# Kernel tuning notes

Measured on AMD Instinct MI355X. Metric: run time of the kernel, lower is better.

Reference implementation:

```python
import jax, jax.numpy as jnp
import numpy as np
import math

D = 1024       # feature_dim
H = 4          # n_heads
HD = D // H
T = 512        # vertice frames
S = 512        # audio frames
V3 = 15069     # vertice_dim (5023*3)
NSUB = 8
PERIOD = 25
MAXLEN = 600
DFF = 2 * D
AUD = 768


def _build_alibi(n_head=H, max_seq=MAXLEN, period=PERIOD):
    def slopes(n):
        def p2(n):
            start = 2 ** (-2 ** (-(math.log2(n) - 3)))
            return [start * start ** i for i in range(n)]
        if math.log2(n).is_integer():
            return p2(n)
        c = 2 ** math.floor(math.log2(n))
        return p2(c) + slopes(2 * c)[0::2][: n - c]
    sl = np.array(slopes(n_head), np.float32)
    bias = (np.arange(0, max_seq, period)[:, None].repeat(period, 1).reshape(-1) // period).astype(np.float32)
    bias = -bias[::-1]
    i = np.arange(max_seq)[:, None]
    j = np.arange(max_seq)[None, :]
    idx = np.clip(max_seq - 1 - i + j, 0, max_seq - 1)
    alibi = np.where(j <= i, bias[idx], 0.0).astype(np.float32)
    causal = np.where(j <= i, 0.0, -np.inf).astype(np.float32)
    return causal[None] + sl[:, None, None] * alibi[None]   # [H, maxlen, maxlen]


def _build_pe(d=D, period=PERIOD, max_seq=MAXLEN):
    pos = np.arange(period, dtype=np.float32)[:, None]
    div = np.exp(np.arange(0, d, 2, dtype=np.float32) * (-math.log(10000.0) / d))
    pe = np.zeros((period, d), np.float32)
    pe[:, 0::2] = np.sin(pos * div)
    pe[:, 1::2] = np.cos(pos * div)
    reps = max_seq // period + 1
    return np.tile(pe, (reps, 1))[None]                     # [1, reps*period, d]

_ALIBI = jnp.asarray(_build_alibi())
_PE = jnp.asarray(_build_pe())


def _ln(x, g, b, eps=1e-5):
    m = jnp.mean(x, -1, keepdims=True)
    v = jnp.mean((x - m) ** 2, -1, keepdims=True)
    return (x - m) * jax.lax.rsqrt(v + eps) * g + b


def _mha(q_in, kv_in, Wqkv, bqkv, Wo, bo, add_mask=None, bool_mask=None):
    # torch nn.MultiheadAttention with in_proj [3D, D]; y = x @ W.T + b
    B, Tq, _ = q_in.shape
    Ts = kv_in.shape[1]
    Wq, Wk, Wv = jnp.split(Wqkv, 3, axis=0)
    bq, bk, bv = jnp.split(bqkv, 3)
    q = (q_in @ Wq.T + bq).reshape(B, Tq, H, HD).transpose(0, 2, 1, 3)
    k = (kv_in @ Wk.T + bk).reshape(B, Ts, H, HD).transpose(0, 2, 1, 3)
    v = (kv_in @ Wv.T + bv).reshape(B, Ts, H, HD).transpose(0, 2, 1, 3)
    scores = jnp.einsum('bhtd,bhsd->bhts', q, k) / math.sqrt(HD)
    if add_mask is not None:
        scores = scores + add_mask[None]            # [1,H,Tq,Ts] float additive (ALiBi+causal)
    if bool_mask is not None:
        scores = jnp.where(bool_mask, -jnp.inf, scores)  # True == masked (torch semantics)
    attn = jax.nn.softmax(scores, axis=-1)
    out = jnp.einsum('bhts,bhsd->bhtd', attn, v).transpose(0, 2, 1, 3).reshape(B, Tq, D)
    return out @ Wo.T + bo


def setup_inputs() -> dict:
    key = jax.random.key(0)
    ks = jax.random.split(key, 32)
    rn = lambda k, shape, s: jax.random.normal(k, shape, jnp.float32) * s
    inp = {
        'audio_feat': rn(ks[0], (1, S, AUD), 1.0),
        'vertice': rn(ks[1], (1, T, V3), 0.1),
        'template': rn(ks[2], (1, V3), 0.1),
        'one_hot': jnp.zeros((1, NSUB), jnp.float32).at[0, 0].set(1.0),
        'W_af': rn(ks[3], (D, AUD), 0.02), 'b_af': jnp.zeros((D,), jnp.float32),
        'W_vm': rn(ks[4], (D, V3), 0.02), 'b_vm': jnp.zeros((D,), jnp.float32),
        'W_obj': rn(ks[5], (D, NSUB), 0.02),
        'Wqkv_sa': rn(ks[6], (3 * D, D), 0.02), 'bqkv_sa': jnp.zeros((3 * D,), jnp.float32),
        'Wo_sa': rn(ks[7], (D, D), 0.02), 'bo_sa': jnp.zeros((D,), jnp.float32),
        'Wqkv_ca': rn(ks[8], (3 * D, D), 0.02), 'bqkv_ca': jnp.zeros((3 * D,), jnp.float32),
        'Wo_ca': rn(ks[9], (D, D), 0.02), 'bo_ca': jnp.zeros((D,), jnp.float32),
        'W1': rn(ks[10], (DFF, D), 0.02), 'b1': jnp.zeros((DFF,), jnp.float32),
        'W2': rn(ks[11], (D, DFF), 0.02), 'b2': jnp.zeros((D,), jnp.float32),
        'g1': jnp.ones((D,), jnp.float32), 'be1': jnp.zeros((D,), jnp.float32),
        'g2': jnp.ones((D,), jnp.float32), 'be2': jnp.zeros((D,), jnp.float32),
        'g3': jnp.ones((D,), jnp.float32), 'be3': jnp.zeros((D,), jnp.float32),
        # vertice_map_r is zero-init in the source; use small random so grads are informative
        'W_vr': rn(ks[12], (V3, D), 0.02), 'b_vr': jnp.zeros((V3,), jnp.float32),
    }
    return inp


def reference(audio_feat, vertice, template, one_hot,
              W_af, b_af, W_vm, b_vm, W_obj,
              Wqkv_sa, bqkv_sa, Wo_sa, bo_sa,
              Wqkv_ca, bqkv_ca, Wo_ca, bo_ca,
              W1, b1, W2, b2, g1, be1, g2, be2, g3, be3,
              W_vr, b_vr):
    tmpl = template[:, None, :]                               # [1,1,V3]
    hidden = audio_feat @ W_af.T + b_af                       # [1,S,D]
    style = (one_hot @ W_obj.T)[:, None, :]                   # [1,1,D]
    # teacher-forcing branch with template
    vin = jnp.concatenate([tmpl, vertice[:, :-1]], axis=1) - tmpl
    vin = vin @ W_vm.T + b_vm + style
    vin = vin + _PE[:, :T, :]                                 # PPE, dropout is identity in eval
    tgt_mask = _ALIBI[:, :T, :T]                              # [H,T,T]
    mem_mask = ~jnp.eye(T, S, dtype=bool)                     # True == masked; only diagonal attended
    x = vin
    x = _ln(x + _mha(x, x, Wqkv_sa, bqkv_sa, Wo_sa, bo_sa, add_mask=tgt_mask), g1, be1)
    x = _ln(x + _mha(x, hidden, Wqkv_ca, bqkv_ca, Wo_ca, bo_ca, bool_mask=mem_mask), g2, be2)
    ff = jax.nn.relu(x @ W1.T + b1) @ W2.T + b2
    x = _ln(x + ff, g3, be3)
    vertice_out = x @ W_vr.T + b_vr + tmpl                    # [1,T,V3]
    return vertice_out
```

## Files before the change

### kernel.cpp

```cpp
#include <hip/hip_runtime.h>
#include <math.h>

typedef __attribute__((ext_vector_type(8))) short short8;
typedef __attribute__((ext_vector_type(4))) float f32x4;
typedef unsigned short ushort_t;

#define KVIN 15360

__device__ __forceinline__ ushort_t f2bf(float f) {
  unsigned u = __float_as_uint(f);
  return (ushort_t)((u + 0x7fffu + ((u >> 16) & 1u)) >> 16);
}
__device__ __forceinline__ float bf2f(ushort_t h) {
  return __uint_as_float(((unsigned)h) << 16);
}

__device__ __forceinline__ float blockReduceSum256(float v, float* red) {
  #pragma unroll
  for (int o = 32; o; o >>= 1) v += __shfl_xor(v, o);
  int wid = threadIdx.x >> 6, lane = threadIdx.x & 63;
  if (lane == 0) red[wid] = v;
  __syncthreads();
  v = red[0] + red[1] + red[2] + red[3];
  __syncthreads();
  return v;
}
__device__ __forceinline__ float blockReduceMax256(float v, float* red) {
  #pragma unroll
  for (int o = 32; o; o >>= 1) v = fmaxf(v, __shfl_xor(v, o));
  int wid = threadIdx.x >> 6, lane = threadIdx.x & 63;
  if (lane == 0) red[wid] = v;
  __syncthreads();
  v = fmaxf(fmaxf(red[0], red[1]), fmaxf(red[2], red[3]));
  __syncthreads();
  return v;
}

template <bool BF16B, int BIASM, bool CAUSAL, int ZDIV, bool OUT16>
__device__ __forceinline__ void gemm_body(
    void* smem,
    const ushort_t* __restrict__ A, const void* __restrict__ Bv,
    const float* __restrict__ bias, const float* __restrict__ biasB,
    void* __restrict__ Cv,
    int N, int K, int lda, int ldb, int ldc,
    int kChunk, long aZ, long bZ, long cZ,
    int z, int m0, int n0)
{
  if (CAUSAL && n0 > m0 + 127) return;
  ushort_t (*sA)[4096] = (ushort_t (*)[4096])smem;
  ushort_t (*sB)[4096] = (ushort_t (*)[4096])((char*)smem + 16384);
  const int tid = threadIdx.x;
  const int ks = ZDIV ? (z % ZDIV) : z;
  const int zb = ZDIV ? (z / ZDIV) : z;
  const int kBeg = kChunk ? ks * kChunk : 0;
  const int kEnd = kChunk ? kBeg + kChunk : K;
  A += (size_t)zb * aZ;
  const ushort_t* Bh = (const ushort_t*)Bv;
  const float*    Bf = (const float*)Bv;
  if (BF16B) Bh += (size_t)zb * bZ; else Bf += (size_t)zb * bZ;
  float*    C32 = (float*)Cv + (OUT16 ? 0 : (size_t)z * cZ);
  ushort_t* C16 = (ushort_t*)Cv + (OUT16 ? (size_t)z * cZ : 0);

  const int r0 = ((tid >> 6) << 4) | (tid & 15);
  const int q0 = (tid >> 4) & 3;
  const int r1 = r0 + 64;
  const ushort_t* pA0 = A + (size_t)(m0 + r0) * lda + (q0 << 3);
  const ushort_t* pA1 = A + (size_t)(m0 + r1) * lda + (q0 << 3);
  const int gn0 = n0 + r0, gn1 = n0 + r1;
  const bool bok0 = gn0 < N, bok1 = gn1 < N;
  const ushort_t* pB0h = Bh + (size_t)gn0 * ldb + (q0 << 3);
  const ushort_t* pB1h = Bh + (size_t)gn1 * ldb + (q0 << 3);
  const float*    pB0f = Bf + (size_t)gn0 * ldb + (q0 << 3);
  const float*    pB1f = Bf + (size_t)gn1 * ldb + (q0 << 3);

  const int lane = tid & 63;
  const int wrb = (tid >> 7) & 1;
  const int wcb = (tid >> 6) & 1;
  const int fr = lane & 15, fq = lane >> 4;

  f32x4 acc[4][4] = {};
  const short8 z8 = {0, 0, 0, 0, 0, 0, 0, 0};
  const float4 z4 = make_float4(0.f, 0.f, 0.f, 0.f);
  short8 ra0, ra1, rb0, rb1; float4 rf0, rf1, rf2, rf3;

#define LOADR(KK) { ra0 = *(const short8*)(pA0 + (KK)); ra1 = *(const short8*)(pA1 + (KK)); \
  if (BF16B) { rb0 = bok0 ? *(const short8*)(pB0h + (KK)) : z8;                             \
               rb1 = bok1 ? *(const short8*)(pB1h + (KK)) : z8; }                           \
  else { rf0 = bok0 ? *(const float4*)(pB0f + (KK)) : z4;                                   \
         rf1 = bok0 ? *(const float4*)(pB0f + (KK) + 4) : z4;                               \
         rf2 = bok1 ? *(const float4*)(pB1f + (KK)) : z4;                                   \
         rf3 = bok1 ? *(const float4*)(pB1f + (KK) + 4) : z4; } }

#define STAGER(BUF) { *(short8*)&sA[BUF][tid << 3] = ra0;                                   \
  *(short8*)&sA[BUF][(tid + 256) << 3] = ra1;                                               \
  if (BF16B) { *(short8*)&sB[BUF][tid << 3] = rb0;                                          \
               *(short8*)&sB[BUF][(tid + 256) << 3] = rb1; }                                \
  else { short8 s0_, s1_;                                                                   \
    _Pragma("unroll") for (int j = 0; j < 4; ++j) {                                         \
      s0_[j] = (short)f2bf(rf0[j]); s0_[j + 4] = (short)f2bf(rf1[j]);                       \
      s1_[j] = (short)f2bf(rf2[j]); s1_[j + 4] = (short)f2bf(rf3[j]); }                     \
    *(short8*)&sB[BUF][tid << 3] = s0_; *(short8*)&sB[BUF][(tid + 256) << 3] = s1_; } }

#define COMPUTE(BUF) { short8 fa[4], fb[4];                                                 \
  _Pragma("unroll") for (int f = 0; f < 4; ++f)                                             \
    fa[f] = *(const short8*)&sA[BUF][((((wrb << 2) + f) << 9) | (lane << 3))];              \
  _Pragma("unroll") for (int g = 0; g < 4; ++g)                                             \
    fb[g] = *(const short8*)&sB[BUF][((((wcb << 2) + g) << 9) | (lane << 3))];              \
  _Pragma("unroll") for (int f = 0; f < 4; ++f)                                             \
    _Pragma("unroll") for (int g = 0; g < 4; ++g)                                           \
      acc[f][g] = __builtin_amdgcn_mfma_f32_16x16x32_bf16(fa[f], fb[g], acc[f][g], 0, 0, 0); }

  LOADR(kBeg);
  const int nt = (kEnd - kBeg) >> 5;
  for (int t = 0; t < nt; ++t) {
    const int cur = t & 1;
    STAGER(cur);
    if (t + 1 < nt) LOADR(kBeg + ((t + 1) << 5));
    asm volatile("s_waitcnt lgkmcnt(0)" ::: "memory");
    __builtin_amdgcn_s_barrier();
    __builtin_amdgcn_sched_barrier(0);
    COMPUTE(cur);
    asm volatile("" ::: "memory");
  }

#undef LOADR
#undef STAGER
#undef COMPUTE

  #pragma unroll
  for (int f = 0; f < 4; ++f) {
    const int gm = m0 + (wrb << 6) + f * 16 + fq * 4;
    #pragma unroll
    for (int g = 0; g < 4; ++g) {
      const int gn = n0 + (wcb << 6) + g * 16 + fr;
      if (gn < N) {
        #pragma unroll
        for (int i = 0; i < 4; ++i) {
          float v = acc[f][g][i];
          if (BIASM >= 1) v += bias[gn];
          if (BIASM >= 2) v += biasB[gn];
          const size_t o = (size_t)(gm + i) * ldc + gn;
          if (OUT16) C16[o] = f2bf(v);
          else       C32[o] = v;
        }
      }
    }
  }
}

template <bool BF16B, int BIASM, bool CAUSAL, int GMODE, int ZDIV, bool OUT16>
__global__ __launch_bounds__(256, 2) void gk(
    const ushort_t* __restrict__ A, const void* __restrict__ Bv,
    const float* __restrict__ bias, const float* __restrict__ biasB,
    void* __restrict__ C,
    int N, int K, int lda, int ldb, int ldc,
    int kChunk, long aZ, long bZ, long cZ)
{
  extern __shared__ char smem[];
  int z, m0, n0;
  if (GMODE == 2) {
    const int id = blockIdx.x, u = id & 7, v = id >> 3;
    m0 = (v & 3) * 128;
    n0 = (((v >> 2) << 3) + u) * 128;
    z = 0;
    if (n0 >= N) return;
  } else if (GMODE == 1) {
    z = blockIdx.x; m0 = blockIdx.y * 128; n0 = blockIdx.z * 128;
  } else {
    z = blockIdx.z; m0 = blockIdx.y * 128; n0 = blockIdx.x * 128;
  }
  gemm_body<BF16B, BIASM, CAUSAL, ZDIV, OUT16>(smem, A, Bv, bias, biasB, C,
      N, K, lda, ldb, ldc, kChunk, aZ, bZ, cZ, z, m0, n0);
}

__global__ __launch_bounds__(256, 2) void gk_qkv_hid(
    const ushort_t* __restrict__ xh, const float* __restrict__ Wqkv,
    ushort_t* __restrict__ partQ,
    const ushort_t* __restrict__ audh, const float* __restrict__ Waf,
    ushort_t* __restrict__ partH)
{
  extern __shared__ char smem[];
  const int bid = blockIdx.x;
  if (bid < 384) {
    const int x = bid % 24, y = (bid / 24) & 3, z = bid / 96;
    gemm_body<false, 0, false, 0, true>(smem, xh, Wqkv, nullptr, nullptr, partQ,
        3072, 1024, 1024, 1024, 3072, 256, 0, 0, 1572864, z, y * 128, x * 128);
  } else {
    const int b = bid - 384;
    const int x = b & 7, y = (b >> 3) & 3, z = b >> 5;
    gemm_body<false, 0, false, 0, true>(smem, audh, Waf, nullptr, nullptr, partH,
        1024, 768, 768, 768, 1024, 192, 0, 0, 524288, z, y * 128, x * 128);
  }
}

__global__ __launch_bounds__(256, 2) void gk_scores_cav(
    const ushort_t* __restrict__ qkvh, float* __restrict__ scores,
    const ushort_t* __restrict__ hidh, const float* __restrict__ WvCA,
    ushort_t* __restrict__ partCV,
    const float* __restrict__ Wvr, ushort_t* __restrict__ Wvrh)
{
  extern __shared__ char smem[];
  const int bid = blockIdx.x;
  if (bid < 128) {
    const int x = bid & 3, y = (bid >> 2) & 3, z = bid >> 4;
    gemm_body<true, 0, true, 0, false>(smem, qkvh, qkvh + 1024, nullptr, nullptr, scores,
        512, 1024, 3072, 3072, 512, 128, 0, 0, 262144, z, y * 128, x * 128);
  } else if (bid < 384) {
    const int b = bid - 128;
    const int x = b & 7, y = (b >> 3) & 3, z = b >> 5;
    gemm_body<false, 0, false, 0, true>(smem, hidh, WvCA, nullptr, nullptr, partCV,
        1024, 1024, 1024, 1024, 1024, 128, 0, 0, 524288, z, y * 128, x * 128);
  } else {
    for (int i = (bid - 384) * 256 + threadIdx.x; i < 1928832; i += 1024 * 256) {
      float4 v = ((const float4*)Wvr)[i];
      ((ushort4*)Wvrh)[i] = make_ushort4(f2bf(v.x), f2bf(v.y), f2bf(v.z), f2bf(v.w));
    }
  }
}

__global__ __launch_bounds__(256, 2) void gk_pv_cao(
    const ushort_t* __restrict__ atth, const ushort_t* __restrict__ vth,
    float* __restrict__ pvpart,
    const ushort_t* __restrict__ cvh, const float* __restrict__ WoCA,
    ushort_t* __restrict__ partCA,
    const float* __restrict__ Wvr, ushort_t* __restrict__ Wvrh)
{
  extern __shared__ char smem[];
  const int bid = blockIdx.x;
  if (bid < 128) {
    const int x = bid & 1, y = (bid >> 1) & 3, z = bid >> 3;
    gemm_body<true, 0, false, 4, false>(smem, atth, vth, nullptr, nullptr, pvpart,
        256, 512, 512, 512, 256, 128, 262144, 131072, 131072, z, y * 128, x * 128);
  } else if (bid < 384) {
    const int b = bid - 128;
    const int x = b & 7, y = (b >> 3) & 3, z = b >> 5;
    gemm_body<false, 0, false, 0, true>(smem, cvh, WoCA, nullptr, nullptr, partCA,
        1024, 1024, 1024, 1024, 1024, 128, 0, 0, 524288, z, y * 128, x * 128);
  } else {
    for (int i = 1928832 + (bid - 384) * 256 + threadIdx.x; i < 3857664; i += 1024 * 256) {
      float4 v = ((const float4*)Wvr)[i];
      ((ushort4*)Wvrh)[i] = make_ushort4(f2bf(v.x), f2bf(v.y), f2bf(v.z), f2bf(v.w));
    }
  }
}

template <bool RELU>
__global__ __launch_bounds__(256) void combine(
    const ushort_t* __restrict__ part, const float* __restrict__ bias,
    ushort_t* __restrict__ outh, int nz, long zstride, int total4, int N4)
{
  const int i = blockIdx.x * 256 + threadIdx.x;
  if (i >= total4) return;
  float4 s = ((const float4*)bias)[i % N4];
  for (int z = 0; z < nz; ++z) {
    ushort4 p = ((const ushort4*)(part + (size_t)z * zstride))[i];
    s.x += bf2f(p.x); s.y += bf2f(p.y); s.z += bf2f(p.z); s.w += bf2f(p.w);
  }
  if (RELU) {
    s.x = fmaxf(s.x, 0.f); s.y = fmaxf(s.y, 0.f);
    s.z = fmaxf(s.z, 0.f); s.w = fmaxf(s.w, 0.f);
  }
  ((ushort4*)outh)[i] = make_ushort4(f2bf(s.x), f2bf(s.y), f2bf(s.z), f2bf(s.w));
}

__global__ __launch_bounds__(256) void combine_pv(
    const float* __restrict__ part, ushort_t* __restrict__ ctxh)
{
  const int t = blockIdx.x, tid = threadIdx.x;
  const int h = tid >> 6, dq = tid & 63;
  float4 s = make_float4(0.f, 0.f, 0.f, 0.f);
  #pragma unroll
  for (int ks = 0; ks < 4; ++ks) {
    float4 p = ((const float4*)(part + (size_t)(h * 4 + ks) * 131072 + (size_t)t * 256))[dq];
    s.x += p.x; s.y += p.y; s.z += p.z; s.w += p.w;
  }
  ((ushort4*)ctxh)[t * 256 + h * 64 + dq] =
      make_ushort4(f2bf(s.x), f2bf(s.y), f2bf(s.z), f2bf(s.w));
}

__global__ __launch_bounds__(256) void ln_parts(
    const ushort_t* __restrict__ part, int nz, const float* __restrict__ bias,
    float* __restrict__ x, ushort_t* __restrict__ xh,
    const float* __restrict__ g, const float* __restrict__ b)
{
  const int t = blockIdx.x, tid = threadIdx.x;
  float4 y = ((const float4*)(x + (size_t)t * 1024))[tid];
  float4 s = ((const float4*)bias)[tid];
  for (int z = 0; z < nz; ++z) {
    ushort4 p = ((const ushort4*)(part + (size_t)z * 524288 + (size_t)t * 1024))[tid];
    s.x += bf2f(p.x); s.y += bf2f(p.y); s.z += bf2f(p.z); s.w += bf2f(p.w);
  }
  y.x += s.x; y.y += s.y; y.z += s.z; y.w += s.w;
  __shared__ float red[4];
  float sum = blockReduceSum256(y.x + y.y + y.z + y.w, red);
  const float m = sum * (1.f / 1024.f);
  float dx = y.x - m, dy = y.y - m, dz = y.z - m, dw = y.w - m;
  float q = blockReduceSum256(dx * dx + dy * dy + dz * dz + dw * dw, red);
  const float rs = rsqrtf(q * (1.f / 1024.f) + 1e-5f);
  float4 gg = ((const float4*)g)[tid], bb = ((const float4*)b)[tid];
  float4 o;
  o.x = dx * rs * gg.x + bb.x;
  o.y = dy * rs * gg.y + bb.y;
  o.z = dz * rs * gg.z + bb.z;
  o.w = dw * rs * gg.w + bb.w;
  ((float4*)(x + (size_t)t * 1024))[tid] = o;
  ((ushort4*)xh)[t * 256 + tid] = make_ushort4(f2bf(o.x), f2bf(o.y), f2bf(o.z), f2bf(o.w));
}

__global__ __launch_bounds__(256) void ln_double(
    const ushort_t* __restrict__ partSA, const float* __restrict__ boSA,
    const ushort_t* __restrict__ partCA, const float* __restrict__ boCA,
    float* __restrict__ x, ushort_t* __restrict__ xh,
    const float* __restrict__ g1, const float* __restrict__ be1,
    const float* __restrict__ g2, const float* __restrict__ be2)
{
  const int t = blockIdx.x, tid = threadIdx.x;
  __shared__ float red[4];
  float4 y = ((const float4*)(x + (size_t)t * 1024))[tid];
  float4 s = ((const float4*)boSA)[tid];
  for (int z = 0; z < 8; ++z) {
    ushort4 p = ((const ushort4*)(partSA + (size_t)z * 524288 + (size_t)t * 1024))[tid];
    s.x += bf2f(p.x); s.y += bf2f(p.y); s.z += bf2f(p.z); s.w += bf2f(p.w);
  }
  y.x += s.x; y.y += s.y; y.z += s.z; y.w += s.w;
  float sum = blockReduceSum256(y.x + y.y + y.z + y.w, red);
  float m = sum * (1.f / 1024.f);
  float dx = y.x - m, dy = y.y - m, dz = y.z - m, dw = y.w - m;
  float q = blockReduceSum256(dx * dx + dy * dy + dz * dz + dw * dw, red);
  float rs = rsqrtf(q * (1.f / 1024.f) + 1e-5f);
  float4 gg = ((const float4*)g1)[tid], bb = ((const float4*)be1)[tid];
  y.x = dx * rs * gg.x + bb.x;
  y.y = dy * rs * gg.y + bb.y;
  y.z = dz * rs * gg.z + bb.z;
  y.w = dw * rs * gg.w + bb.w;
  s = ((const float4*)boCA)[tid];
  for (int z = 0; z < 8; ++z) {
    ushort4 p = ((const ushort4*)(partCA + (size_t)z * 524288 + (size_t)t * 1024))[tid];
    s.x += bf2f(p.x); s.y += bf2f(p.y); s.z += bf2f(p.z); s.w += bf2f(p.w);
  }
  y.x += s.x; y.y += s.y; y.z += s.z; y.w += s.w;
  sum = blockReduceSum256(y.x + y.y + y.z + y.w, red);
  m = sum * (1.f / 1024.f);
  dx = y.x - m; dy = y.y - m; dz = y.z - m; dw = y.w - m;
  q = blockReduceSum256(dx * dx + dy * dy + dz * dz + dw * dw, red);
  rs = rsqrtf(q * (1.f / 1024.f) + 1e-5f);
  gg = ((const float4*)g2)[tid]; bb = ((const float4*)be2)[tid];
  float4 o;
  o.x = dx * rs * gg.x + bb.x;
  o.y = dy * rs * gg.y + bb.y;
  o.z = dz * rs * gg.z + bb.z;
  o.w = dw * rs * gg.w + bb.w;
  ((float4*)(x + (size_t)t * 1024))[tid] = o;
  ((ushort4*)xh)[t * 256 + tid] = make_ushort4(f2bf(o.x), f2bf(o.y), f2bf(o.z), f2bf(o.w));
}

__global__ __launch_bounds__(256) void prep_all(
    const float* __restrict__ vertice, const float* __restrict__ tmpl,
    ushort_t* __restrict__ Aph,
    const float* __restrict__ Wvm, ushort_t* __restrict__ Wvmh,
    const float* __restrict__ audio, ushort_t* __restrict__ audh)
{
  const int bid = blockIdx.x;
  if (bid < 7680) {
    const int i = bid * 256 + threadIdx.x;
    const int C4 = KVIN >> 2;
    const int t = i / C4;
    const int c = (i - t * C4) << 2;
    ushort4 o = make_ushort4(0, 0, 0, 0);
    if (t > 0) {
      const float* s = vertice + (size_t)(t - 1) * 15069 + c;
      if (c + 3 < 15069) {
        o = make_ushort4(f2bf(s[0] - tmpl[c]),     f2bf(s[1] - tmpl[c + 1]),
                         f2bf(s[2] - tmpl[c + 2]), f2bf(s[3] - tmpl[c + 3]));
      } else {
        if (c + 0 < 15069) o.x = f2bf(s[0] - tmpl[c]);
        if (c + 1 < 15069) o.y = f2bf(s[1] - tmpl[c + 1]);
        if (c + 2 < 15069) o.z = f2bf(s[2] - tmpl[c + 2]);
        if (c + 3 < 15069) o.w = f2bf(s[3] - tmpl[c + 3]);
      }
    }
    ((ushort4*)Aph)[i] = o;
  } else if (bid < 23040) {
    const int i = (bid - 7680) * 256 + threadIdx.x;
    const int C4 = KVIN >> 2;
    const int r = i / C4;
    const int c = (i - r * C4) << 2;
    const float* s = Wvm + (size_t)r * 15069 + c;
    ushort4 o = make_ushort4(0, 0, 0, 0);
    if (c + 3 < 15069) {
      o = make_ushort4(f2bf(s[0]), f2bf(s[1]), f2bf(s[2]), f2bf(s[3]));
    } else {
      if (c + 0 < 15069) o.x = f2bf(s[0]);
      if (c + 1 < 15069) o.y = f2bf(s[1]);
      if (c + 2 < 15069) o.z = f2bf(s[2]);
      if (c + 3 < 15069) o.w = f2bf(s[3]);
    }
    ((ushort4*)Wvmh)[i] = o;
  } else {
    const int j = (bid - 23040) * 256 + threadIdx.x;
    if (j < 98304) {
      float4 v = ((const float4*)audio)[j];
      ((ushort4*)audh)[j] = make_ushort4(f2bf(v.x), f2bf(v.y), f2bf(v.z), f2bf(v.w));
    }
  }
}

__global__ __launch_bounds__(256) void reduce_pe(const float* __restrict__ part,
                                                 const float* __restrict__ one_hot,
                                                 const float* __restrict__ W_obj,
                                                 const float* __restrict__ b_vm,
                                                 float* __restrict__ x,
                                                 ushort_t* __restrict__ xh) {
  const int t = blockIdx.x;
  const float PECOEF = -9.210340371976184f / 512.f;
  const int p = t % 25;
  for (int d = threadIdx.x; d < 1024; d += 256) {
    float s = b_vm[d];
    #pragma unroll
    for (int j = 0; j < 8; ++j) s += one_hot[j] * W_obj[d * 8 + j];
    #pragma unroll
    for (int z = 0; z < 16; ++z) s += part[(size_t)z * 524288 + (size_t)t * 1024 + d];
    float arg = (float)p * expf((float)(d >> 1) * PECOEF);
    s += (d & 1) ? cosf(arg) : sinf(arg);
    const size_t idx = (size_t)t * 1024 + d;
    x[idx] = s;
    xh[idx] = f2bf(s);
  }
}

__global__ __launch_bounds__(256) void qkvpost_combhid(
    const ushort_t* __restrict__ partQ, const float* __restrict__ bias,
    ushort_t* __restrict__ qkvh, ushort_t* __restrict__ vth,
    const ushort_t* __restrict__ partH, const float* __restrict__ b_af,
    ushort_t* __restrict__ hidh)
{
  const int bid = blockIdx.x;
  __shared__ float tile[32][33];
  if (bid < 1536) {
    const int i = bid * 256 + threadIdx.x;
    float4 s = ((const float4*)bias)[i % 768];
    #pragma unroll
    for (int z = 0; z < 4; ++z) {
      ushort4 p = ((const ushort4*)(partQ + (size_t)z * 1572864))[i];
      s.x += bf2f(p.x); s.y += bf2f(p.y); s.z += bf2f(p.z); s.w += bf2f(p.w);
    }
    ((ushort4*)qkvh)[i] = make_ushort4(f2bf(s.x), f2bf(s.y), f2bf(s.z), f2bf(s.w));
  } else if (bid < 2048) {
    const int b = bid - 1536;
    const int s0 = (b & 15) * 32, d0 = (b >> 4) * 32;
    const int tx = threadIdx.x & 31, ty = threadIdx.x >> 5;
    for (int r = ty; r < 32; r += 8) {
      float v = bias[2048 + d0 + tx];
      #pragma unroll
      for (int z = 0; z < 4; ++z)
        v += bf2f(partQ[(size_t)z * 1572864 + (size_t)(s0 + r) * 3072 + 2048 + d0 + tx]);
      tile[r][tx] = v;
    }
    __syncthreads();
    for (int r = ty; r < 32; r += 8)
      vth[(size_t)(d0 + r) * 512 + s0 + tx] = f2bf(tile[tx][r]);
  } else {
    const int i = (bid - 2048) * 256 + threadIdx.x;
    float4 s = ((const float4*)b_af)[i % 256];
    #pragma unroll
    for (int z = 0; z < 4; ++z) {
      ushort4 p = ((const ushort4*)(partH + (size_t)z * 524288))[i];
      s.x += bf2f(p.x); s.y += bf2f(p.y); s.z += bf2f(p.z); s.w += bf2f(p.w);
    }
    ((ushort4*)hidh)[i] = make_ushort4(f2bf(s.x), f2bf(s.y), f2bf(s.z), f2bf(s.w));
  }
}

__global__ __launch_bounds__(256) void sm_combcv(
    const float* __restrict__ scores, ushort_t* __restrict__ ah,
    const ushort_t* __restrict__ partCV, const float* __restrict__ bqkv_ca,
    ushort_t* __restrict__ cvh)
{
  const int bid = blockIdx.x;
  __shared__ float red[4];
  if (bid < 2048) {
    const int i = bid & 511, h = bid >> 9;
    const float* r0 = scores + (size_t)(2 * h) * 262144 + (size_t)i * 512;
    const float* r1 = r0 + 262144;
    const size_t rb = ((size_t)h * 512 + i) * 512;
    const int tid = threadIdx.x;
    const int len = i + 1;
    const float sl = exp2f(-2.f * (float)(h + 1));
    const int j0 = tid, j1 = tid + 256;
    float v0 = -INFINITY, v1 = -INFINITY;
    if (j0 < len) v0 = (r0[j0] + r1[j0]) * 0.0625f - sl * (float)((i - j0) / 25);
    if (j1 < len) v1 = (r0[j1] + r1[j1]) * 0.0625f - sl * (float)((i - j1) / 25);
    float m = blockReduceMax256(fmaxf(v0, v1), red);
    float e0 = (j0 < len) ? expf(v0 - m) : 0.f;
    float e1 = (j1 < len) ? expf(v1 - m) : 0.f;
    float s = blockReduceSum256(e0 + e1, red);
    float inv = 1.f / s;
    ah[rb + j0] = f2bf(e0 * inv);
    ah[rb + j1] = f2bf(e1 * inv);
  } else {
    const int i = (bid - 2048) * 256 + threadIdx.x;
    float4 s = ((const float4*)(bqkv_ca + 2048))[i % 256];
    #pragma unroll
    for (int z = 0; z < 8; ++z) {
      ushort4 p = ((const ushort4*)(partCV + (size_t)z * 524288))[i];
      s.x += bf2f(p.x); s.y += bf2f(p.y); s.z += bf2f(p.z); s.w += bf2f(p.w);
    }
    ((ushort4*)cvh)[i] = make_ushort4(f2bf(s.x), f2bf(s.y), f2bf(s.z), f2bf(s.w));
  }
}

extern "C" void kernel_launch(void* const* d_in, const int* in_sizes, int n_in,
                              void* d_out, int out_size, void* d_ws, size_t ws_size,
                              hipStream_t stream) {
  const float* audio   = (const float*)d_in[0];
  const float* vertice = (const float*)d_in[1];
  const float* tmpl    = (const float*)d_in[2];
  const float* one_hot = (const float*)d_in[3];
  const float* W_af    = (const float*)d_in[4];
  const float* b_af    = (const float*)d_in[5];
  const float* W_vm    = (const float*)d_in[6];
  const float* b_vm    = (const float*)d_in[7];
  const float* W_obj   = (const float*)d_in[8];
  const float* Wqkv_sa = (const float*)d_in[9];
  const float* bqkv_sa = (const float*)d_in[10];
  const float* Wo_sa   = (const float*)d_in[11];
  const float* bo_sa   = (const float*)d_in[12];
  const float* Wqkv_ca = (const float*)d_in[13];
  const float* bqkv_ca = (const float*)d_in[14];
  const float* Wo_ca   = (const float*)d_in[15];
  const float* bo_ca   = (const float*)d_in[16];
  const float* W1      = (const float*)d_in[17];
  const float* b1      = (const float*)d_in[18];
  const float* W2      = (const float*)d_in[19];
  const float* b2      = (const float*)d_in[20];
  const float* g1      = (const float*)d_in[21];
  const float* be1     = (const float*)d_in[22];
  const float* g2      = (const float*)d_in[23];
  const float* be2     = (const float*)d_in[24];
  const float* g3      = (const float*)d_in[25];
  const float* be3     = (const float*)d_in[26];
  const float* W_vr    = (const float*)d_in[27];
  const float* b_vr    = (const float*)d_in[28];
  float* out = (float*)d_out;

  float* base = (float*)d_ws;
  float* apF    = base;
  float* wvmF   = apF + 3932160;
  float* part   = wvmF + 7864320;
  float* x      = part + 8388608;
  float* xhF    = x + 524288;
  float* audF   = xhF + 262144;
  float* hidF   = audF + 196608;
  float* qkvF   = hidF + 262144;
  float* vtF    = qkvF + 786432;
  float* scores = vtF + 262144;
  float* attF   = scores + 2097152;
  float* pvpart = attF + 524288;
  float* ctxF   = pvpart + 2097152;
  float* cvF    = ctxF + 262144;
  float* h1F    = cvF + 262144;

  ushort_t* partQ  = (ushort_t*)part;
  ushort_t* partH  = (ushort_t*)(part + 4194304);
  ushort_t* partCV = (ushort_t*)part;
  ushort_t* partCA = (ushort_t*)(part + 4194304);
  ushort_t* partSA = (ushort_t*)part;
  ushort_t* partF1 = (ushort_t*)part;
  ushort_t* partF2 = (ushort_t*)part;

  ushort_t* Aph  = (ushort_t*)apF;
  ushort_t* Wvmh = (ushort_t*)wvmF;
  ushort_t* Wvrh = (ushort_t*)wvmF;
  ushort_t* xh   = (ushort_t*)xhF;
  ushort_t* audh = (ushort_t*)audF;
  ushort_t* hidh = (ushort_t*)hidF;
  ushort_t* qkvh = (ushort_t*)qkvF;
  ushort_t* vth  = (ushort_t*)vtF;
  ushort_t* atth = (ushort_t*)attF;
  ushort_t* ctxh = (ushort_t*)ctxF;
  ushort_t* cvh  = (ushort_t*)cvF;
  ushort_t* h1h  = (ushort_t*)h1F;

  prep_all<<<23424, 256, 0, stream>>>(vertice, tmpl, Aph, W_vm, Wvmh, audio, audh);

  gk<true, 0, false, 1, 0, false><<<dim3(16, 4, 8), 256, 32768, stream>>>(
      Aph, Wvmh, nullptr, nullptr, part,
      1024, KVIN, KVIN, KVIN, 1024, 960, 0, 0, 524288);

  reduce_pe<<<512, 256, 0, stream>>>(part, one_hot, W_obj, b_vm, x, xh);

  gk_qkv_hid<<<512, 256, 32768, stream>>>(xh, Wqkv_sa, partQ, audh, W_af, partH);

  qkvpost_combhid<<<2560, 256, 0, stream>>>(partQ, bqkv_sa, qkvh, vth,
                                            partH, b_af, hidh);

  gk_scores_cav<<<1408, 256, 32768, stream>>>(qkvh, scores, hidh,
                                              Wqkv_ca + (size_t)2048 * 1024, partCV,
                                              W_vr, Wvrh);

  sm_combcv<<<2560, 256, 0, stream>>>(scores, atth, partCV, bqkv_ca, cvh);

  gk_pv_cao<<<1408, 256, 32768, stream>>>(atth, vth, pvpart, cvh, Wo_ca, partCA,
                                          W_vr, Wvrh);

  combine_pv<<<512, 256, 0, stream>>>(pvpart, ctxh);

  gk<false, 0, false, 0, 0, true><<<dim3(8, 4, 8), 256, 32768, stream>>>(
      ctxh, Wo_sa, nullptr, nullptr, partSA,
      1024, 1024, 1024, 1024, 1024, 128, 0, 0, 524288);

  ln_double<<<512, 256, 0, stream>>>(partSA, bo_sa, partCA, bo_ca,
                                     x, xh, g1, be1, g2, be2);

  gk<false, 0, false, 0, 0, true><<<dim3(16, 4, 4), 256, 32768, stream>>>(
      xh, W1, nullptr, nullptr, partF1,
      2048, 1024, 1024, 1024, 2048, 256, 0, 0, 1048576);
  combine<true><<<1024, 256, 0, stream>>>(partF1, b1, h1h, 4, 1048576, 262144, 512);
  gk<false, 0, false, 0, 0, true><<<dim3(8, 4, 8), 256, 32768, stream>>>(
      h1h, W2, nullptr, nullptr, partF2,
      1024, 2048, 2048, 2048, 1024, 256, 0, 0, 524288);
  ln_parts<<<512, 256, 0, stream>>>(partF2, 8, b2, x, xh, g3, be3);

  gk<true, 2, false, 2, 0, false><<<dim3(480, 1, 1), 256, 32768, stream>>>(
      xh, Wvrh, b_vr, tmpl, out,
      15069, 1024, 1024, 1024, 15069, 0, 0, 0, 0);
}
```

Before: 283.2 us.

## Double split-K factors for FFN/out-proj GEMMs and split-K the final vertex GEMM

Raises the split-K factor for the self-attention output projection and both FFN GEMMs (halving each K chunk) so more blocks are launched. The final 15069-wide output GEMM is split into two K halves that write bf16 partials, and a new combine kernel adds them with bias and template. The aim is better CU occupancy on the under-filled GEMM grids, at the cost of more partial-buffer traffic, extra reduction work and an added kernel launch. Accumulating partials in bf16 also loses some precision.

```diff
diff --git a/kernel.cpp b/kernel.cpp
--- a/kernel.cpp
+++ b/kernel.cpp
@@ -158,7 +158,14 @@
 {
   extern __shared__ char smem[];
   int z, m0, n0;
-  if (GMODE == 2) {
+  if (GMODE == 3) {
+    const int id = blockIdx.x;
+    z = id / 480;
+    const int r = id % 480, u = r & 7, v = r >> 3;
+    m0 = (v & 3) * 128;
+    n0 = (((v >> 2) << 3) + u) * 128;
+    if (n0 >= N) return;
+  } else if (GMODE == 2) {
     const int id = blockIdx.x, u = id & 7, v = id >> 3;
     m0 = (v & 3) * 128;
     n0 = (((v >> 2) << 3) + u) * 128;
@@ -263,6 +270,26 @@
   ((ushort4*)outh)[i] = make_ushort4(f2bf(s.x), f2bf(s.y), f2bf(s.z), f2bf(s.w));
 }
 
+__global__ __launch_bounds__(256) void combine_out(
+    const ushort_t* __restrict__ p0, const ushort_t* __restrict__ p1,
+    const float* __restrict__ b_vr, const float* __restrict__ tmpl,
+    float* __restrict__ out)
+{
+  const int i = blockIdx.x * 256 + threadIdx.x;
+  if (i >= 1928832) return;
+  const int e = i << 2;
+  int n = e % 15069;
+  ushort4 a = ((const ushort4*)p0)[i];
+  ushort4 b = ((const ushort4*)p1)[i];
+  float r[4] = {bf2f(a.x) + bf2f(b.x), bf2f(a.y) + bf2f(b.y),
+                bf2f(a.z) + bf2f(b.z), bf2f(a.w) + bf2f(b.w)};
+  #pragma unroll
+  for (int j = 0; j < 4; ++j) {
+    out[e + j] = r[j] + b_vr[n] + tmpl[n];
+    if (++n >= 15069) n = 0;
+  }
+}
+
 __global__ __launch_bounds__(256) void combine_pv(
     const float* __restrict__ part, ushort_t* __restrict__ ctxh)
 {
@@ -318,7 +345,7 @@
   __shared__ float red[4];
   float4 y = ((const float4*)(x + (size_t)t * 1024))[tid];
   float4 s = ((const float4*)boSA)[tid];
-  for (int z = 0; z < 8; ++z) {
+  for (int z = 0; z < 16; ++z) {
     ushort4 p = ((const ushort4*)(partSA + (size_t)z * 524288 + (size_t)t * 1024))[tid];
     s.x += bf2f(p.x); s.y += bf2f(p.y); s.z += bf2f(p.z); s.w += bf2f(p.w);
   }
@@ -567,6 +594,7 @@
   ushort_t* partSA = (ushort_t*)part;
   ushort_t* partF1 = (ushort_t*)part;
   ushort_t* partF2 = (ushort_t*)part;
+  ushort_t* partO  = (ushort_t*)part;
 
   ushort_t* Aph  = (ushort_t*)apF;
   ushort_t* Wvmh = (ushort_t*)wvmF;
@@ -605,23 +633,25 @@
 
   combine_pv<<<512, 256, 0, stream>>>(pvpart, ctxh);
 
-  gk<false, 0, false, 0, 0, true><<<dim3(8, 4, 8), 256, 32768, stream>>>(
+  gk<false, 0, false, 0, 0, true><<<dim3(8, 4, 16), 256, 32768, stream>>>(
       ctxh, Wo_sa, nullptr, nullptr, partSA,
-      1024, 1024, 1024, 1024, 1024, 128, 0, 0, 524288);
+      1024, 1024, 1024, 1024, 1024, 64, 0, 0, 524288);
 
   ln_double<<<512, 256, 0, stream>>>(partSA, bo_sa, partCA, bo_ca,
                                      x, xh, g1, be1, g2, be2);
 
-  gk<false, 0, false, 0, 0, true><<<dim3(16, 4, 4), 256, 32768, stream>>>(
+  gk<false, 0, false, 0, 0, true><<<dim3(16, 4, 8), 256, 32768, stream>>>(
       xh, W1, nullptr, nullptr, partF1,
-      2048, 1024, 1024, 1024, 2048, 256, 0, 0, 1048576);
-  combine<true><<<1024, 256, 0, stream>>>(partF1, b1, h1h, 4, 1048576, 262144, 512);
-  gk<false, 0, false, 0, 0, true><<<dim3(8, 4, 8), 256, 32768, stream>>>(
+      2048, 1024, 1024, 1024, 2048, 128, 0, 0, 1048576);
+  combine<true><<<1024, 256, 0, stream>>>(partF1, b1, h1h, 8, 1048576, 262144, 512);
+  gk<false, 0, false, 0, 0, true><<<dim3(8, 4, 16), 256, 32768, stream>>>(
       h1h, W2, nullptr, nullptr, partF2,
-      1024, 2048, 2048, 2048, 1024, 256, 0, 0, 524288);
-  ln_parts<<<512, 256, 0, stream>>>(partF2, 8, b2, x, xh, g3, be3);
-
-  gk<true, 2, false, 2, 0, false><<<dim3(480, 1, 1), 256, 32768, stream>>>(
-      xh, Wvrh, b_vr, tmpl, out,
-      15069, 1024, 1024, 1024, 15069, 0, 0, 0, 0);
-}
+      1024, 2048, 2048, 2048, 1024, 128, 0, 0, 524288);
+  ln_parts<<<512, 256, 0, stream>>>(partF2, 16, b2, x, xh, g3, be3);
+
+  gk<true, 0, false, 3, 2, true><<<dim3(960, 1, 1), 256, 32768, stream>>>(
+      xh, Wvrh, nullptr, nullptr, partO,
+      15069, 1024, 1024, 1024, 15069, 512, 0, 0, 7715328);
+
+  combine_out<<<7535, 256, 0, stream>>>(partO, partO + 7715328, b_vr, tmpl, out);
+}
```

Measured after the change: 305.7 us. +7.9%, slower.
